# Optimization experiments

Measured on AMD Instinct MI355X. Metric: run time of the kernel, lower is better.

Reference implementation:

```python
import jax, jax.numpy as jnp
import numpy as np
import math

B, S, H = 4, 4096, 64
WINDOW = 2


def setup_inputs() -> dict:
    key = jax.random.key(0)
    ks = jax.random.split(key, 7)
    s = 0.05
    return {
        "feature": jax.random.normal(ks[0], (B, S, H), dtype=jnp.float32),
        "Wq": jax.random.normal(ks[1], (H, H), dtype=jnp.float32) * s,
        "bq": jax.random.normal(ks[2], (H,), dtype=jnp.float32) * s,
        "Wk": jax.random.normal(ks[3], (H, H), dtype=jnp.float32) * s,
        "bk": jax.random.normal(ks[4], (H,), dtype=jnp.float32) * s,
        "Wv": jax.random.normal(ks[5], (H, H), dtype=jnp.float32) * s,
        "bv": jax.random.normal(ks[6], (H,), dtype=jnp.float32) * s,
    }


def reference(feature, Wq, bq, Wk, bk, Wv, bv):
    b, seq, d_k = feature.shape
    # torch nn.Linear: y = x @ W.T + b
    q = feature @ Wq.T + bq  # [B,S,H]
    k = feature @ Wk.T + bk
    v = feature @ Wv.T + bv

    # banded 0/1 mask, |i-j| <= window, then softmax over the FULL row
    # (faithful to the original: zeros outside the band also get exp(0)=1 weight)
    idx = jnp.arange(seq)
    band = (jnp.abs(idx[:, None] - idx[None, :]) <= WINDOW).astype(jnp.float32)  # [S,S]
    weights = jax.nn.softmax(band, axis=-1)  # [S,S]

    # locally-averaged K: weights @ k, shared across batch
    mixed_k = jnp.einsum('st,bth->bsh', weights, k)  # [B,S,H]
    scores = jnp.einsum('bsh,bth->bst', q, mixed_k) / math.sqrt(d_k)  # [B,S,S]
    attn = jax.nn.softmax(scores, axis=-1)
    out = jnp.einsum('bst,bth->bsh', attn, v)  # [B,S,H]
    return out
```

## Files before the change

### kernel.cpp

```cpp
#include <hip/hip_runtime.h>
#include <hip/hip_bf16.h>
#include <math.h>

#define SEQ 4096
#define HD  64
#define NBATCH 4

#define EM1   1.71828182845904523536f
#define INVD5 (1.0f/(4096.f + 5.f*EM1))
#define INVD4 (1.0f/(4096.f + 4.f*EM1))
#define INVD3 (1.0f/(4096.f + 3.f*EM1))

typedef __attribute__((ext_vector_type(8))) short short8;
typedef __attribute__((ext_vector_type(4))) float f32x4;

__device__ __forceinline__ f32x4 mfma16(short8 a, short8 b, f32x4 c) {
    return __builtin_amdgcn_mfma_f32_16x16x32_bf16(a, b, c, 0, 0, 0);
}

__device__ __forceinline__ short bfs(float x) {
    __hip_bfloat16 h = __float2bfloat16(x);
    return *(short*)&h;
}

__device__ __forceinline__ short8 pack8(float4 a, float4 b) {
    short8 r;
    r[0] = bfs(a.x); r[1] = bfs(a.y); r[2] = bfs(a.z); r[3] = bfs(a.w);
    r[4] = bfs(b.x); r[5] = bfs(b.y); r[6] = bfs(b.z); r[7] = bfs(b.w);
    return r;
}

__device__ __forceinline__ float blo(unsigned v) { return __uint_as_float(v << 16); }
__device__ __forceinline__ float bhi(unsigned v) { return __uint_as_float(v & 0xffff0000u); }
__device__ __forceinline__ float b2f(__hip_bfloat16 h) { return __bfloat162float(h); }

__global__ __launch_bounds__(256) void wpack_kernel(
    const float* __restrict__ Wq, const float* __restrict__ Wk,
    const float* __restrict__ Wv, __hip_bfloat16* __restrict__ Wb,
    float* __restrict__ Mfull)
{
    const int blk = blockIdx.x, tid = threadIdx.x;
    if (blk >= 3) {
        float4 z = make_float4(0.f, 0.f, 0.f, 0.f);
        *(float4*)&Mfull[(blk - 3) * 1024 + tid * 4] = z;
        return;
    }
    const float* W = (blk == 0) ? Wq : (blk == 1) ? Wk : Wv;
    const float s = (blk == 0) ? 0.125f : 1.f;
    const float* src = W + tid * 16;
    float4 a0 = *(const float4*)(src);
    float4 a1 = *(const float4*)(src + 4);
    float4 a2 = *(const float4*)(src + 8);
    float4 a3 = *(const float4*)(src + 12);
    a0.x*=s; a0.y*=s; a0.z*=s; a0.w*=s;
    a1.x*=s; a1.y*=s; a1.z*=s; a1.w*=s;
    a2.x*=s; a2.y*=s; a2.z*=s; a2.w*=s;
    a3.x*=s; a3.y*=s; a3.z*=s; a3.w*=s;
    __hip_bfloat16* dst = Wb + blk * 4096 + tid * 16;
    *(short8*)(dst)     = pack8(a0, a1);
    *(short8*)(dst + 8) = pack8(a2, a3);
}

__global__ __launch_bounds__(128) void proj_kernel(
    const float* __restrict__ feat, const __hip_bfloat16* __restrict__ Wb,
    const float* __restrict__ bq, const float* __restrict__ bk,
    const float* __restrict__ bv,
    __hip_bfloat16* __restrict__ qsb, __hip_bfloat16* __restrict__ ktb,
    __hip_bfloat16* __restrict__ vtb,
    float* __restrict__ kpart, float* __restrict__ vpart)
{
    __shared__ __hip_bfloat16 tscr[64 * 72];
    __shared__ float kred[2][64];

    const int tid  = threadIdx.x;
    const int wave = tid >> 6, lane = tid & 63;
    const int quad = lane >> 4, ln = lane & 15;
    const int R0 = blockIdx.x * 32;
    const int b  = R0 >> 12;
    const int t0 = R0 & (SEQ - 1);

    short8 af0, af1;
    {
        const float* fp = feat + (size_t)(R0 + wave * 16 + ln) * HD + quad * 8;
        af0 = pack8(*(const float4*)(fp),      *(const float4*)(fp + 4));
        af1 = pack8(*(const float4*)(fp + 32), *(const float4*)(fp + 36));
    }

    const float* Bs[3] = {bq, bk, bv};

    #pragma unroll
    for (int m = 0; m < 3; ++m) {
        const __hip_bfloat16* W = Wb + m * 4096;
        const float* bias = Bs[m];
        #pragma unroll
        for (int ct = 0; ct < 4; ++ct) {
            const int col = ct * 16 + ln;
            const __hip_bfloat16* wp = W + col * 64 + quad * 8;
            short8 b0 = *(const short8*)(wp);
            short8 b1 = *(const short8*)(wp + 32);
            f32x4 c = {};
            c = mfma16(af0, b0, c);
            c = mfma16(af1, b1, c);

            if (m == 0) {
                const float bl = bias[col] * 0.125f;
                #pragma unroll
                for (int r = 0; r < 4; ++r)
                    qsb[(size_t)(R0 + wave * 16 + quad * 4 + r) * HD + col] =
                        __float2bfloat16(c[r] + bl);
            } else {
                const float bl = bias[col];
                float tot = c[0] + c[1] + c[2] + c[3];
                tot += __shfl_xor(tot, 16);
                tot += __shfl_xor(tot, 32);
                if (quad == 0) kred[wave][col] = tot;
                #pragma unroll
                for (int r = 0; r < 4; ++r)
                    tscr[col * 72 + wave * 16 + quad * 4 + r] =
                        __float2bfloat16(c[r] + bl);
            }
        }
        if (m > 0) {
            __syncthreads();
            if (tid < 64)
                ((m == 1) ? kpart : vpart)[(size_t)blockIdx.x * 64 + tid] =
                    kred[0][tid] + kred[1][tid] + 32.f * bias[tid];
            __hip_bfloat16* dst = (m == 1) ? ktb : vtb;
            #pragma unroll
            for (int i = 0; i < 2; ++i) {
                const int tsk = i * 128 + tid;
                const int hh = tsk >> 2, c8 = tsk & 3;
                short8 vv = *(const short8*)&tscr[hh * 72 + c8 * 8];
                *(short8*)(dst + ((size_t)(b * HD + hh)) * SEQ + t0 + c8 * 8) = vv;
            }
            __syncthreads();
        }
    }
}

__global__ __launch_bounds__(256) void mkernel(
    const __hip_bfloat16* __restrict__ ktb, const __hip_bfloat16* __restrict__ vtb,
    const float* __restrict__ kpart, const float* __restrict__ vpart,
    float* __restrict__ Mfull, float* __restrict__ Mcorr,
    float* __restrict__ mktotF, float* __restrict__ Vtot)
{
    __shared__ float vws[64 * 38];
    __shared__ __hip_bfloat16 lvt[64 * 40];
    __shared__ float scr[4][64];
    __shared__ float ktl[64], vtl[64];
    __shared__ float lc[4][64], vv_e[4][64];

    const int tid = threadIdx.x;

    if (blockIdx.y == 4) {
        if (blockIdx.x >= 16) return;
        const int b = blockIdx.x >> 2, slab = blockIdx.x & 3;
        if (slab == 2) return;
        const int h = tid & 63, g = tid >> 6;

        if (slab == 0 || slab == 3) {
            float kp = 0.f;
            for (int j = 0; j < 32; ++j)
                kp += kpart[(size_t)(b * 128 + g * 32 + j) * 64 + h];
            scr[g][h] = kp;
            __syncthreads();
            if (tid < 64) ktl[tid] = scr[0][tid] + scr[1][tid] + scr[2][tid] + scr[3][tid];
        }
        if (slab == 0) {
            __syncthreads();
            if (tid < 64) {
                const int hh = tid;
                const float kt = ktl[hh];
                const __hip_bfloat16* kr = ktb + (size_t)(b * 64 + hh) * SEQ;
                const float e0 = b2f(kr[0]), e1 = b2f(kr[1]), e2 = b2f(kr[2]), e3 = b2f(kr[3]);
                const float f0 = b2f(kr[SEQ-4]), f1 = b2f(kr[SEQ-3]);
                const float f2 = b2f(kr[SEQ-2]), f3 = b2f(kr[SEQ-1]);
                const float Sint = 5.f*kt - 4.f*e0 - 3.f*e1 - 2.f*e2 - e3
                                 - f0 - 2.f*f1 - 3.f*f2 - 4.f*f3;
                const float SlocD = Sint * INVD5
                                  + (e0+e1+e2 + f1+f2+f3) * INVD3
                                  + (e0+e1+e2+e3 + f0+f1+f2+f3) * INVD4;
                mktotF[b * 64 + hh] =
                    kt * (4092.f*INVD5 + 2.f*INVD4 + 2.f*INVD3) + EM1 * SlocD;
            }
        } else if (slab == 1) {
            float vp = 0.f;
            for (int j = 0; j < 32; ++j)
                vp += vpart[(size_t)(b * 128 + g * 32 + j) * 64 + h];
            scr[g][h] = vp;
            __syncthreads();
            if (tid < 64)
                Vtot[b * 64 + tid] = scr[0][tid] + scr[1][tid] + scr[2][tid] + scr[3][tid];
        } else {
            __syncthreads();
            {
                float vp = 0.f;
                for (int j = 0; j < 32; ++j)
                    vp += vpart[(size_t)(b * 128 + g * 32 + j) * 64 + h];
                scr[g][h] = vp;
            }
            __syncthreads();
            if (tid < 64) vtl[tid] = scr[0][tid] + scr[1][tid] + scr[2][tid] + scr[3][tid];
            if (tid < 64) {
                const int hh = tid;
                const __hip_bfloat16* kr = ktb + (size_t)(b * 64 + hh) * SEQ;
                const float e0 = b2f(kr[0]), e1 = b2f(kr[1]), e2 = b2f(kr[2]), e3 = b2f(kr[3]);
                const float f0 = b2f(kr[SEQ-4]), f1 = b2f(kr[SEQ-3]);
                const float f2 = b2f(kr[SEQ-2]), f3 = b2f(kr[SEQ-1]);
                lc[0][hh] = e0 + e1 + e2;
                lc[1][hh] = e0 + e1 + e2 + e3;
                lc[2][hh] = f0 + f1 + f2 + f3;
                lc[3][hh] = f1 + f2 + f3;
                const __hip_bfloat16* vr = vtb + (size_t)(b * 64 + hh) * SEQ;
                vv_e[0][hh] = b2f(vr[0]);
                vv_e[1][hh] = b2f(vr[1]);
                vv_e[2][hh] = b2f(vr[SEQ-2]);
                vv_e[3][hh] = b2f(vr[SEQ-1]);
            }
            __syncthreads();
            const float dd3 = INVD3 - INVD5, dd4 = INVD4 - INVD5;
            const int h1 = tid >> 2;
            const float l0 = lc[0][h1], l1 = lc[1][h1], l2 = lc[2][h1], l3 = lc[3][h1];
            const float kt1 = ktl[h1];
            #pragma unroll
            for (int j = 0; j < 16; ++j) {
                const int h2 = (tid & 3) * 16 + j;
                const float VD = INVD5 * vtl[h2]
                               + dd3 * (vv_e[0][h2] + vv_e[3][h2])
                               + dd4 * (vv_e[1][h2] + vv_e[2][h2]);
                Mcorr[(size_t)(b * 64 + h1) * 64 + h2] =
                    EM1 * (dd3 * (l0 * vv_e[0][h2] + l3 * vv_e[3][h2])
                         + dd4 * (l1 * vv_e[1][h2] + l2 * vv_e[2][h2]))
                    + kt1 * VD;
            }
        }
        return;
    }

    const int b = blockIdx.y, chunk = blockIdx.x;
    const int t0 = chunk * 32;

    for (int i = tid; i < 64 * 18; i += 256) {
        const int r = i / 18, c = i - r * 18;
        const int gt = t0 - 2 + c * 2;
        unsigned val = 0;
        if (gt >= 0 && gt <= SEQ - 2)
            val = *(const unsigned*)(vtb + (size_t)(b * 64 + r) * SEQ + gt);
        vws[r * 38 + c * 2]     = blo(val);
        vws[r * 38 + c * 2 + 1] = bhi(val);
    }
    __syncthreads();

    {
        const int h = tid & 63, g = tid >> 6;
        float w[12];
        #pragma unroll
        for (int j = 0; j < 12; ++j) w[j] = vws[h * 38 + g * 8 + j];
        short8 o;
        #pragma unroll
        for (int i = 0; i < 8; ++i)
            o[i] = bfs(w[i] + w[i+1] + w[i+2] + w[i+3] + w[i+4]);
        *(short8*)&lvt[h * 40 + g * 8] = o;
    }
    __syncthreads();

    const int wave = tid >> 6, lane = tid & 63, quad = lane >> 4, ln = lane & 15;
    short8 a = *(const short8*)(ktb + (size_t)(b * 64 + wave * 16 + ln) * SEQ
                                + t0 + quad * 8);
    f32x4 acc[4] = {};
    #pragma unroll
    for (int ct = 0; ct < 4; ++ct) {
        short8 bb = *(const short8*)&lvt[(ct * 16 + ln) * 40 + quad * 8];
        acc[ct] = mfma16(a, bb, acc[ct]);
    }
    float* mf = Mfull + b * 4096;
    #pragma unroll
    for (int ct = 0; ct < 4; ++ct)
        #pragma unroll
        for (int r = 0; r < 4; ++r)
            atomicAdd(&mf[(wave * 16 + quad * 4 + r) * 64 + ct * 16 + ln],
                      acc[ct][r]);
}

__global__ __launch_bounds__(256) void out_kernel(
    const __hip_bfloat16* __restrict__ qsb, const float* __restrict__ Mfull,
    const float* __restrict__ Mcorr, const float* __restrict__ mktotF,
    const float* __restrict__ Vtot, float* __restrict__ out)
{
    __shared__ __hip_bfloat16 tscr[64 * 72];

    const int tid  = threadIdx.x;
    const int wave = tid >> 6, lane = tid & 63;
    const int quad = lane >> 4, ln = lane & 15;
    const int R0 = blockIdx.x * 64;
    const int b  = R0 >> 12;

    {
        const int h2 = tid & 63, seg = tid >> 6;
        #pragma unroll
        for (int j = 0; j < 16; ++j) {
            const int h1 = seg * 16 + j;
            const float m = (EM1 * INVD5) * Mfull[b * 4096 + h1 * 64 + h2]
                          + Mcorr[(size_t)(b * 64 + h1) * 64 + h2];
            tscr[h2 * 72 + h1] = __float2bfloat16(m);
        }
    }
    __syncthreads();

    short8 qa0, qa1;
    {
        const __hip_bfloat16* qp = qsb + (size_t)(R0 + wave * 16 + ln) * HD + quad * 8;
        qa0 = *(const short8*)qp;
        qa1 = *(const short8*)(qp + 32);
    }
    short8 mk0, mk1;
    #pragma unroll
    for (int j = 0; j < 8; ++j) {
        mk0[j] = bfs(mktotF[b * 64 + quad * 8 + j]);
        mk1[j] = bfs(mktotF[b * 64 + 32 + quad * 8 + j]);
    }

    f32x4 acc[4];
    #pragma unroll
    for (int ct = 0; ct < 4; ++ct) {
        short8 b0 = *(const short8*)&tscr[(ct * 16 + ln) * 72 + quad * 8];
        short8 b1 = *(const short8*)&tscr[(ct * 16 + ln) * 72 + 32 + quad * 8];
        f32x4 c = {};
        c = mfma16(qa0, b0, c);
        c = mfma16(qa1, b1, c);
        acc[ct] = c;
    }
    f32x4 accd = {};
    accd = mfma16(qa0, mk0, accd);
    accd = mfma16(qa1, mk1, accd);

    float vt[4];
    #pragma unroll
    for (int ct = 0; ct < 4; ++ct) vt[ct] = Vtot[b * 64 + ct * 16 + ln];

    float inv[4];
    #pragma unroll
    for (int r = 0; r < 4; ++r) inv[r] = 1.f / (4096.f + accd[r]);

    #pragma unroll
    for (int ct = 0; ct < 4; ++ct)
        #pragma unroll
        for (int r = 0; r < 4; ++r)
            out[(size_t)(R0 + wave * 16 + quad * 4 + r) * HD + ct * 16 + ln] =
                (vt[ct] + acc[ct][r]) * inv[r];
}

extern "C" void kernel_launch(void* const* d_in, const int* in_sizes, int n_in,
                              void* d_out, int out_size, void* d_ws, size_t ws_size,
                              hipStream_t stream)
{
    const float* feat = (const float*)d_in[0];
    const float* Wq = (const float*)d_in[1];
    const float* bq = (const float*)d_in[2];
    const float* Wk = (const float*)d_in[3];
    const float* bk = (const float*)d_in[4];
    const float* Wv = (const float*)d_in[5];
    const float* bv = (const float*)d_in[6];
    float* out = (float*)d_out;

    char* ws = (char*)d_ws;
    __hip_bfloat16* qsb    = (__hip_bfloat16*)(ws + 0);
    __hip_bfloat16* ktb    = (__hip_bfloat16*)(ws + (2u << 20));
    __hip_bfloat16* vtb    = (__hip_bfloat16*)(ws + (4u << 20));
    float*          kpart  = (float*)(ws + (6u << 20));
    float*          vpart  = (float*)(ws + (6u << 20) + 131072);
    float*          Mfull  = (float*)(ws + (6u << 20) + 262144);
    float*          Mcorr  = (float*)(ws + (6u << 20) + 327680);
    float*          mktotF = (float*)(ws + (6u << 20) + 393216);
    float*          Vtot   = (float*)(ws + (6u << 20) + 394240);
    __hip_bfloat16* Wb     = (__hip_bfloat16*)(ws + (6u << 20) + 395264);

    wpack_kernel<<<dim3(19), dim3(256), 0, stream>>>(Wq, Wk, Wv, Wb, Mfull);
    proj_kernel<<<dim3(512), dim3(128), 0, stream>>>(
        feat, Wb, bq, bk, bv, qsb, ktb, vtb, kpart, vpart);
    mkernel<<<dim3(128, 5), dim3(256), 0, stream>>>(
        ktb, vtb, kpart, vpart, Mfull, Mcorr, mktotF, Vtot);
    out_kernel<<<dim3(256), dim3(256), 0, stream>>>(
        qsb, Mfull, Mcorr, mktotF, Vtot, out);
}
```

Baseline: 91.88 us.

## Fuse per-chunk K^T·localV products into projection kernel, replace atomics with partial reduction

The projection kernel now computes each 32-row chunk's K^T times the locally summed V directly from shared memory, loading two halo rows of features to build the V window. Each chunk writes its partial matrix to a buffer, so the transposed K/V round-trip through global memory and the float atomics into Mfull go away. A new reduction kernel sums the partials, and the edge-correction terms are simplified and folded into the output via a ktot·VD term. The cost is more partial-matrix traffic (bf16 Mpart) and an extra reduction pass.

```diff
diff --git a/kernel.cpp b/kernel.cpp
--- a/kernel.cpp
+++ b/kernel.cpp
@@ -30,21 +30,13 @@
     return r;
 }
 
-__device__ __forceinline__ float blo(unsigned v) { return __uint_as_float(v << 16); }
-__device__ __forceinline__ float bhi(unsigned v) { return __uint_as_float(v & 0xffff0000u); }
 __device__ __forceinline__ float b2f(__hip_bfloat16 h) { return __bfloat162float(h); }
 
 __global__ __launch_bounds__(256) void wpack_kernel(
     const float* __restrict__ Wq, const float* __restrict__ Wk,
-    const float* __restrict__ Wv, __hip_bfloat16* __restrict__ Wb,
-    float* __restrict__ Mfull)
+    const float* __restrict__ Wv, __hip_bfloat16* __restrict__ Wb)
 {
     const int blk = blockIdx.x, tid = threadIdx.x;
-    if (blk >= 3) {
-        float4 z = make_float4(0.f, 0.f, 0.f, 0.f);
-        *(float4*)&Mfull[(blk - 3) * 1024 + tid * 4] = z;
-        return;
-    }
     const float* W = (blk == 0) ? Wq : (blk == 1) ? Wk : Wv;
     const float s = (blk == 0) ? 0.125f : 1.f;
     const float* src = W + tid * 16;
@@ -61,16 +53,19 @@
     *(short8*)(dst + 8) = pack8(a2, a3);
 }
 
-__global__ __launch_bounds__(128) void proj_kernel(
+__global__ __launch_bounds__(128) void projm_kernel(
     const float* __restrict__ feat, const __hip_bfloat16* __restrict__ Wb,
     const float* __restrict__ bq, const float* __restrict__ bk,
     const float* __restrict__ bv,
-    __hip_bfloat16* __restrict__ qsb, __hip_bfloat16* __restrict__ ktb,
-    __hip_bfloat16* __restrict__ vtb,
-    float* __restrict__ kpart, float* __restrict__ vpart)
-{
-    __shared__ __hip_bfloat16 tscr[64 * 72];
+    __hip_bfloat16* __restrict__ qsb, float* __restrict__ kpart,
+    float* __restrict__ vpart, __hip_bfloat16* __restrict__ Mpart,
+    float* __restrict__ kedge)
+{
+    __shared__ __hip_bfloat16 kT[64 * 40];
+    __shared__ __hip_bfloat16 vT[64 * 40];
+    __shared__ __hip_bfloat16 lvt[64 * 40];
     __shared__ float kred[2][64];
+    __shared__ float vred[2][64];
 
     const int tid  = threadIdx.x;
     const int wave = tid >> 6, lane = tid & 63;
@@ -78,12 +73,27 @@
     const int R0 = blockIdx.x * 32;
     const int b  = R0 >> 12;
     const int t0 = R0 & (SEQ - 1);
+    const int chunk = blockIdx.x & 127;
 
     short8 af0, af1;
     {
         const float* fp = feat + (size_t)(R0 + wave * 16 + ln) * HD + quad * 8;
         af0 = pack8(*(const float4*)(fp),      *(const float4*)(fp + 4));
         af1 = pack8(*(const float4*)(fp + 32), *(const float4*)(fp + 36));
+    }
+
+    short8 hf0, hf1;
+    const bool hflag = (wave == 0) ? (t0 > 0) : (t0 < SEQ - 32);
+    {
+        const int hrow = (wave == 0) ? (t0 - 2 + ln) : (t0 + 32 + ln);
+        if (ln < 2 && hflag) {
+            const float* fp = feat + ((size_t)(b << 12) + hrow) * HD + quad * 8;
+            hf0 = pack8(*(const float4*)(fp),      *(const float4*)(fp + 4));
+            hf1 = pack8(*(const float4*)(fp + 32), *(const float4*)(fp + 36));
+        } else {
+            #pragma unroll
+            for (int j = 0; j < 8; ++j) { hf0[j] = 0; hf1[j] = 0; }
+        }
     }
 
     const float* Bs[3] = {bq, bk, bv};
@@ -108,7 +118,7 @@
                 for (int r = 0; r < 4; ++r)
                     qsb[(size_t)(R0 + wave * 16 + quad * 4 + r) * HD + col] =
                         __float2bfloat16(c[r] + bl);
-            } else {
+            } else if (m == 1) {
                 const float bl = bias[col];
                 float tot = c[0] + c[1] + c[2] + c[3];
                 tot += __shfl_xor(tot, 16);
@@ -116,227 +126,195 @@
                 if (quad == 0) kred[wave][col] = tot;
                 #pragma unroll
                 for (int r = 0; r < 4; ++r)
-                    tscr[col * 72 + wave * 16 + quad * 4 + r] =
+                    kT[col * 40 + wave * 16 + quad * 4 + r] =
                         __float2bfloat16(c[r] + bl);
+            } else {
+                const float bl = bias[col];
+                float tot = c[0] + c[1] + c[2] + c[3];
+                tot += __shfl_xor(tot, 16);
+                tot += __shfl_xor(tot, 32);
+                if (quad == 0) vred[wave][col] = tot;
+                #pragma unroll
+                for (int r = 0; r < 4; ++r)
+                    vT[col * 40 + 2 + wave * 16 + quad * 4 + r] =
+                        __float2bfloat16(c[r] + bl);
+                f32x4 hc = {};
+                hc = mfma16(hf0, b0, hc);
+                hc = mfma16(hf1, b1, hc);
+                if (quad == 0) {
+                    const int base = (wave == 0) ? 0 : 34;
+                    vT[col * 40 + base]     = __float2bfloat16(hflag ? hc[0] + bl : 0.f);
+                    vT[col * 40 + base + 1] = __float2bfloat16(hflag ? hc[1] + bl : 0.f);
+                }
             }
         }
-        if (m > 0) {
-            __syncthreads();
-            if (tid < 64)
-                ((m == 1) ? kpart : vpart)[(size_t)blockIdx.x * 64 + tid] =
-                    kred[0][tid] + kred[1][tid] + 32.f * bias[tid];
-            __hip_bfloat16* dst = (m == 1) ? ktb : vtb;
+    }
+    __syncthreads();
+
+    if (tid < 64) {
+        kpart[(size_t)blockIdx.x * 64 + tid] =
+            kred[0][tid] + kred[1][tid] + 32.f * bk[tid];
+        vpart[(size_t)blockIdx.x * 64 + tid] =
+            vred[0][tid] + vred[1][tid] + 32.f * bv[tid];
+    }
+
+    {
+        const int h = tid & 63;
+        const int tb = wave * 16;
+        float w[21];
+        #pragma unroll
+        for (int j = 0; j < 21; ++j) w[j] = b2f(vT[h * 40 + tb + j]);
+        #pragma unroll
+        for (int i = 0; i < 16; ++i)
+            lvt[h * 40 + tb + i] =
+                __float2bfloat16(w[i] + w[i+1] + w[i+2] + w[i+3] + w[i+4]);
+    }
+
+    if (chunk == 0) {
+        #pragma unroll
+        for (int i = 0; i < 2; ++i) {
+            const int idx = i * 128 + tid;
+            const int t = idx >> 6, h = idx & 63;
+            kedge[b * 512 + t * 64 + h] = b2f(kT[h * 40 + t]);
+        }
+    } else if (chunk == 127) {
+        #pragma unroll
+        for (int i = 0; i < 2; ++i) {
+            const int idx = i * 128 + tid;
+            const int t = idx >> 6, h = idx & 63;
+            kedge[b * 512 + (4 + t) * 64 + h] = b2f(kT[h * 40 + 28 + t]);
+        }
+    }
+    __syncthreads();
+
+    __hip_bfloat16* mp = Mpart + (size_t)(b * 128 + chunk) * 4096;
+    #pragma unroll
+    for (int p = 0; p < 2; ++p) {
+        const int strip = wave * 2 + p;
+        short8 a = *(const short8*)&kT[(strip * 16 + ln) * 40 + quad * 8];
+        #pragma unroll
+        for (int ct = 0; ct < 4; ++ct) {
+            short8 bb = *(const short8*)&lvt[(ct * 16 + ln) * 40 + quad * 8];
+            f32x4 acc = {};
+            acc = mfma16(a, bb, acc);
             #pragma unroll
-            for (int i = 0; i < 2; ++i) {
-                const int tsk = i * 128 + tid;
-                const int hh = tsk >> 2, c8 = tsk & 3;
-                short8 vv = *(const short8*)&tscr[hh * 72 + c8 * 8];
-                *(short8*)(dst + ((size_t)(b * HD + hh)) * SEQ + t0 + c8 * 8) = vv;
-            }
-            __syncthreads();
-        }
-    }
-}
-
-__global__ __launch_bounds__(256) void mkernel(
-    const __hip_bfloat16* __restrict__ ktb, const __hip_bfloat16* __restrict__ vtb,
-    const float* __restrict__ kpart, const float* __restrict__ vpart,
-    float* __restrict__ Mfull, float* __restrict__ Mcorr,
-    float* __restrict__ mktotF, float* __restrict__ Vtot)
-{
-    __shared__ float vws[64 * 38];
-    __shared__ __hip_bfloat16 lvt[64 * 40];
-    __shared__ float scr[4][64];
-    __shared__ float ktl[64], vtl[64];
-    __shared__ float lc[4][64], vv_e[4][64];
-
+            for (int r = 0; r < 4; ++r)
+                mp[(strip * 16 + quad * 4 + r) * 64 + ct * 16 + ln] =
+                    __float2bfloat16(acc[r]);
+        }
+    }
+}
+
+__global__ __launch_bounds__(256) void redprep_kernel(
+    const __hip_bfloat16* __restrict__ Mpart, const float* __restrict__ kpart,
+    const float* __restrict__ vpart, const float* __restrict__ kedge,
+    __hip_bfloat16* __restrict__ MTm, float* __restrict__ mktotF,
+    float* __restrict__ ktotF, float* __restrict__ VDs,
+    float* __restrict__ VtotF)
+{
+    __shared__ float red[4][64];
+    __shared__ float red2[4][64];
+    const int b = blockIdx.y, x = blockIdx.x;
     const int tid = threadIdx.x;
-
-    if (blockIdx.y == 4) {
-        if (blockIdx.x >= 16) return;
-        const int b = blockIdx.x >> 2, slab = blockIdx.x & 3;
-        if (slab == 2) return;
-        const int h = tid & 63, g = tid >> 6;
-
-        if (slab == 0 || slab == 3) {
-            float kp = 0.f;
-            for (int j = 0; j < 32; ++j)
-                kp += kpart[(size_t)(b * 128 + g * 32 + j) * 64 + h];
-            scr[g][h] = kp;
-            __syncthreads();
-            if (tid < 64) ktl[tid] = scr[0][tid] + scr[1][tid] + scr[2][tid] + scr[3][tid];
-        }
-        if (slab == 0) {
-            __syncthreads();
-            if (tid < 64) {
-                const int hh = tid;
-                const float kt = ktl[hh];
-                const __hip_bfloat16* kr = ktb + (size_t)(b * 64 + hh) * SEQ;
-                const float e0 = b2f(kr[0]), e1 = b2f(kr[1]), e2 = b2f(kr[2]), e3 = b2f(kr[3]);
-                const float f0 = b2f(kr[SEQ-4]), f1 = b2f(kr[SEQ-3]);
-                const float f2 = b2f(kr[SEQ-2]), f3 = b2f(kr[SEQ-1]);
-                const float Sint = 5.f*kt - 4.f*e0 - 3.f*e1 - 2.f*e2 - e3
-                                 - f0 - 2.f*f1 - 3.f*f2 - 4.f*f3;
-                const float SlocD = Sint * INVD5
-                                  + (e0+e1+e2 + f1+f2+f3) * INVD3
-                                  + (e0+e1+e2+e3 + f0+f1+f2+f3) * INVD4;
-                mktotF[b * 64 + hh] =
-                    kt * (4092.f*INVD5 + 2.f*INVD4 + 2.f*INVD3) + EM1 * SlocD;
-            }
-        } else if (slab == 1) {
-            float vp = 0.f;
-            for (int j = 0; j < 32; ++j)
-                vp += vpart[(size_t)(b * 128 + g * 32 + j) * 64 + h];
-            scr[g][h] = vp;
-            __syncthreads();
-            if (tid < 64)
-                Vtot[b * 64 + tid] = scr[0][tid] + scr[1][tid] + scr[2][tid] + scr[3][tid];
-        } else {
-            __syncthreads();
-            {
-                float vp = 0.f;
-                for (int j = 0; j < 32; ++j)
-                    vp += vpart[(size_t)(b * 128 + g * 32 + j) * 64 + h];
-                scr[g][h] = vp;
-            }
-            __syncthreads();
-            if (tid < 64) vtl[tid] = scr[0][tid] + scr[1][tid] + scr[2][tid] + scr[3][tid];
-            if (tid < 64) {
-                const int hh = tid;
-                const __hip_bfloat16* kr = ktb + (size_t)(b * 64 + hh) * SEQ;
-                const float e0 = b2f(kr[0]), e1 = b2f(kr[1]), e2 = b2f(kr[2]), e3 = b2f(kr[3]);
-                const float f0 = b2f(kr[SEQ-4]), f1 = b2f(kr[SEQ-3]);
-                const float f2 = b2f(kr[SEQ-2]), f3 = b2f(kr[SEQ-1]);
-                lc[0][hh] = e0 + e1 + e2;
-                lc[1][hh] = e0 + e1 + e2 + e3;
-                lc[2][hh] = f0 + f1 + f2 + f3;
-                lc[3][hh] = f1 + f2 + f3;
-                const __hip_bfloat16* vr = vtb + (size_t)(b * 64 + hh) * SEQ;
-                vv_e[0][hh] = b2f(vr[0]);
-                vv_e[1][hh] = b2f(vr[1]);
-                vv_e[2][hh] = b2f(vr[SEQ-2]);
-                vv_e[3][hh] = b2f(vr[SEQ-1]);
-            }
-            __syncthreads();
-            const float dd3 = INVD3 - INVD5, dd4 = INVD4 - INVD5;
-            const int h1 = tid >> 2;
-            const float l0 = lc[0][h1], l1 = lc[1][h1], l2 = lc[2][h1], l3 = lc[3][h1];
-            const float kt1 = ktl[h1];
-            #pragma unroll
-            for (int j = 0; j < 16; ++j) {
-                const int h2 = (tid & 3) * 16 + j;
-                const float VD = INVD5 * vtl[h2]
-                               + dd3 * (vv_e[0][h2] + vv_e[3][h2])
-                               + dd4 * (vv_e[1][h2] + vv_e[2][h2]);
-                Mcorr[(size_t)(b * 64 + h1) * 64 + h2] =
-                    EM1 * (dd3 * (l0 * vv_e[0][h2] + l3 * vv_e[3][h2])
-                         + dd4 * (l1 * vv_e[1][h2] + l2 * vv_e[2][h2]))
-                    + kt1 * VD;
-            }
-        }
+    const int g = tid >> 6, h2 = tid & 63;
+
+    if (x < 64) {
+        const int h1 = x;
+        float s = 0.f;
+        for (int c = g * 32; c < g * 32 + 32; ++c)
+            s += b2f(Mpart[(size_t)(b * 128 + c) * 4096 + h1 * 64 + h2]);
+        red[g][h2] = s;
+        __syncthreads();
+        if (tid < 64)
+            MTm[(size_t)b * 4096 + tid * 64 + h1] = __float2bfloat16(
+                (EM1 * INVD5) * (red[0][tid] + red[1][tid] + red[2][tid] + red[3][tid]));
         return;
     }
 
-    const int b = blockIdx.y, chunk = blockIdx.x;
-    const int t0 = chunk * 32;
-
-    for (int i = tid; i < 64 * 18; i += 256) {
-        const int r = i / 18, c = i - r * 18;
-        const int gt = t0 - 2 + c * 2;
-        unsigned val = 0;
-        if (gt >= 0 && gt <= SEQ - 2)
-            val = *(const unsigned*)(vtb + (size_t)(b * 64 + r) * SEQ + gt);
-        vws[r * 38 + c * 2]     = blo(val);
-        vws[r * 38 + c * 2 + 1] = bhi(val);
+    {
+        float kp = 0.f, vp = 0.f;
+        for (int j = 0; j < 32; ++j) {
+            kp += kpart[(size_t)(b * 128 + g * 32 + j) * 64 + h2];
+            vp += vpart[(size_t)(b * 128 + g * 32 + j) * 64 + h2];
+        }
+        red[g][h2] = kp;
+        red2[g][h2] = vp;
     }
     __syncthreads();
-
-    {
-        const int h = tid & 63, g = tid >> 6;
-        float w[12];
-        #pragma unroll
-        for (int j = 0; j < 12; ++j) w[j] = vws[h * 38 + g * 8 + j];
-        short8 o;
-        #pragma unroll
-        for (int i = 0; i < 8; ++i)
-            o[i] = bfs(w[i] + w[i+1] + w[i+2] + w[i+3] + w[i+4]);
-        *(short8*)&lvt[h * 40 + g * 8] = o;
-    }
-    __syncthreads();
-
-    const int wave = tid >> 6, lane = tid & 63, quad = lane >> 4, ln = lane & 15;
-    short8 a = *(const short8*)(ktb + (size_t)(b * 64 + wave * 16 + ln) * SEQ
-                                + t0 + quad * 8);
-    f32x4 acc[4] = {};
-    #pragma unroll
-    for (int ct = 0; ct < 4; ++ct) {
-        short8 bb = *(const short8*)&lvt[(ct * 16 + ln) * 40 + quad * 8];
-        acc[ct] = mfma16(a, bb, acc[ct]);
-    }
-    float* mf = Mfull + b * 4096;
-    #pragma unroll
-    for (int ct = 0; ct < 4; ++ct)
-        #pragma unroll
-        for (int r = 0; r < 4; ++r)
-            atomicAdd(&mf[(wave * 16 + quad * 4 + r) * 64 + ct * 16 + ln],
-                      acc[ct][r]);
-}
-
-__global__ __launch_bounds__(256) void out_kernel(
-    const __hip_bfloat16* __restrict__ qsb, const float* __restrict__ Mfull,
-    const float* __restrict__ Mcorr, const float* __restrict__ mktotF,
-    const float* __restrict__ Vtot, float* __restrict__ out)
-{
-    __shared__ __hip_bfloat16 tscr[64 * 72];
-
-    const int tid  = threadIdx.x;
-    const int wave = tid >> 6, lane = tid & 63;
-    const int quad = lane >> 4, ln = lane & 15;
-    const int R0 = blockIdx.x * 64;
-    const int b  = R0 >> 12;
-
-    {
-        const int h2 = tid & 63, seg = tid >> 6;
-        #pragma unroll
-        for (int j = 0; j < 16; ++j) {
-            const int h1 = seg * 16 + j;
-            const float m = (EM1 * INVD5) * Mfull[b * 4096 + h1 * 64 + h2]
-                          + Mcorr[(size_t)(b * 64 + h1) * 64 + h2];
-            tscr[h2 * 72 + h1] = __float2bfloat16(m);
-        }
-    }
-    __syncthreads();
+    if (tid < 64) {
+        const int hh = tid;
+        const float kt = red[0][hh] + red[1][hh] + red[2][hh] + red[3][hh];
+        const float vt = red2[0][hh] + red2[1][hh] + red2[2][hh] + red2[3][hh];
+        const float e0 = kedge[b * 512 + 0 * 64 + hh];
+        const float e1 = kedge[b * 512 + 1 * 64 + hh];
+        const float e2 = kedge[b * 512 + 2 * 64 + hh];
+        const float e3 = kedge[b * 512 + 3 * 64 + hh];
+        const float f0 = kedge[b * 512 + 4 * 64 + hh];
+        const float f1 = kedge[b * 512 + 5 * 64 + hh];
+        const float f2 = kedge[b * 512 + 6 * 64 + hh];
+        const float f3 = kedge[b * 512 + 7 * 64 + hh];
+        const float Sint = 5.f*kt - 4.f*e0 - 3.f*e1 - 2.f*e2 - e3
+                         - f0 - 2.f*f1 - 3.f*f2 - 4.f*f3;
+        const float SlocD = Sint * INVD5
+                          + (e0+e1+e2 + f1+f2+f3) * INVD3
+                          + (e0+e1+e2+e3 + f0+f1+f2+f3) * INVD4;
+        mktotF[b * 64 + hh] = kt * (4092.f*INVD5 + 2.f*INVD4 + 2.f*INVD3) + EM1 * SlocD;
+        ktotF[b * 64 + hh]  = kt;
+        VDs[b * 64 + hh]    = INVD5 * vt;
+        VtotF[b * 64 + hh]  = vt;
+    }
+}
+
+__global__ __launch_bounds__(64) void out_kernel(
+    const __hip_bfloat16* __restrict__ qsb, const __hip_bfloat16* __restrict__ MTm,
+    const float* __restrict__ mktotF, const float* __restrict__ ktotF,
+    const float* __restrict__ VDs, const float* __restrict__ VtotF,
+    float* __restrict__ out)
+{
+    const int tid = threadIdx.x;
+    const int quad = tid >> 4, ln = tid & 15;
+    const int R0 = blockIdx.x * 16;
+    const int b = R0 >> 12;
 
     short8 qa0, qa1;
     {
-        const __hip_bfloat16* qp = qsb + (size_t)(R0 + wave * 16 + ln) * HD + quad * 8;
+        const __hip_bfloat16* qp = qsb + (size_t)(R0 + ln) * HD + quad * 8;
         qa0 = *(const short8*)qp;
         qa1 = *(const short8*)(qp + 32);
     }
-    short8 mk0, mk1;
-    #pragma unroll
-    for (int j = 0; j < 8; ++j) {
-        mk0[j] = bfs(mktotF[b * 64 + quad * 8 + j]);
-        mk1[j] = bfs(mktotF[b * 64 + 32 + quad * 8 + j]);
-    }
-
+
+    const __hip_bfloat16* mtb = MTm + (size_t)b * 4096;
     f32x4 acc[4];
     #pragma unroll
     for (int ct = 0; ct < 4; ++ct) {
-        short8 b0 = *(const short8*)&tscr[(ct * 16 + ln) * 72 + quad * 8];
-        short8 b1 = *(const short8*)&tscr[(ct * 16 + ln) * 72 + 32 + quad * 8];
+        short8 b0 = *(const short8*)(mtb + (ct * 16 + ln) * 64 + quad * 8);
+        short8 b1 = *(const short8*)(mtb + (ct * 16 + ln) * 64 + 32 + quad * 8);
         f32x4 c = {};
         c = mfma16(qa0, b0, c);
         c = mfma16(qa1, b1, c);
         acc[ct] = c;
     }
-    f32x4 accd = {};
+
+    short8 mk0, mk1, kt0, kt1;
+    #pragma unroll
+    for (int j = 0; j < 8; ++j) {
+        mk0[j] = bfs(mktotF[b * 64 + quad * 8 + j]);
+        mk1[j] = bfs(mktotF[b * 64 + 32 + quad * 8 + j]);
+        kt0[j] = bfs(ktotF[b * 64 + quad * 8 + j]);
+        kt1[j] = bfs(ktotF[b * 64 + 32 + quad * 8 + j]);
+    }
+    f32x4 accd = {}, acck = {};
     accd = mfma16(qa0, mk0, accd);
     accd = mfma16(qa1, mk1, accd);
-
-    float vt[4];
-    #pragma unroll
-    for (int ct = 0; ct < 4; ++ct) vt[ct] = Vtot[b * 64 + ct * 16 + ln];
+    acck = mfma16(qa0, kt0, acck);
+    acck = mfma16(qa1, kt1, acck);
+
+    float vt[4], vd[4];
+    #pragma unroll
+    for (int ct = 0; ct < 4; ++ct) {
+        vt[ct] = VtotF[b * 64 + ct * 16 + ln];
+        vd[ct] = VDs[b * 64 + ct * 16 + ln];
+    }
 
     float inv[4];
     #pragma unroll
@@ -346,8 +324,8 @@
     for (int ct = 0; ct < 4; ++ct)
         #pragma unroll
         for (int r = 0; r < 4; ++r)
-            out[(size_t)(R0 + wave * 16 + quad * 4 + r) * HD + ct * 16 + ln] =
-                (vt[ct] + acc[ct][r]) * inv[r];
+            out[(size_t)(R0 + quad * 4 + r) * HD + ct * 16 + ln] =
+                (vt[ct] + acc[ct][r] + acck[r] * vd[ct]) * inv[r];
 }
 
 extern "C" void kernel_launch(void* const* d_in, const int* in_sizes, int n_in,
@@ -365,21 +343,22 @@
 
     char* ws = (char*)d_ws;
     __hip_bfloat16* qsb    = (__hip_bfloat16*)(ws + 0);
-    __hip_bfloat16* ktb    = (__hip_bfloat16*)(ws + (2u << 20));
-    __hip_bfloat16* vtb    = (__hip_bfloat16*)(ws + (4u << 20));
+    __hip_bfloat16* Mpart  = (__hip_bfloat16*)(ws + (2u << 20));
     float*          kpart  = (float*)(ws + (6u << 20));
     float*          vpart  = (float*)(ws + (6u << 20) + 131072);
-    float*          Mfull  = (float*)(ws + (6u << 20) + 262144);
-    float*          Mcorr  = (float*)(ws + (6u << 20) + 327680);
-    float*          mktotF = (float*)(ws + (6u << 20) + 393216);
-    float*          Vtot   = (float*)(ws + (6u << 20) + 394240);
-    __hip_bfloat16* Wb     = (__hip_bfloat16*)(ws + (6u << 20) + 395264);
-
-    wpack_kernel<<<dim3(19), dim3(256), 0, stream>>>(Wq, Wk, Wv, Wb, Mfull);
-    proj_kernel<<<dim3(512), dim3(128), 0, stream>>>(
-        feat, Wb, bq, bk, bv, qsb, ktb, vtb, kpart, vpart);
-    mkernel<<<dim3(128, 5), dim3(256), 0, stream>>>(
-        ktb, vtb, kpart, vpart, Mfull, Mcorr, mktotF, Vtot);
-    out_kernel<<<dim3(256), dim3(256), 0, stream>>>(
-        qsb, Mfull, Mcorr, mktotF, Vtot, out);
-}
+    float*          kedge  = (float*)(ws + (6u << 20) + 262144);
+    __hip_bfloat16* MTm    = (__hip_bfloat16*)(ws + (6u << 20) + 270336);
+    float*          mktotF = (float*)(ws + (6u << 20) + 303104);
+    float*          ktotF  = (float*)(ws + (6u << 20) + 304128);
+    float*          VDs    = (float*)(ws + (6u << 20) + 305152);
+    float*          VtotF  = (float*)(ws + (6u << 20) + 306176);
+    __hip_bfloat16* Wb     = (__hip_bfloat16*)(ws + (6u << 20) + 307200);
+
+    wpack_kernel<<<dim3(3), dim3(256), 0, stream>>>(Wq, Wk, Wv, Wb);
+    projm_kernel<<<dim3(512), dim3(128), 0, stream>>>(
+        feat, Wb, bq, bk, bv, qsb, kpart, vpart, Mpart, kedge);
+    redprep_kernel<<<dim3(65, NBATCH), dim3(256), 0, stream>>>(
+        Mpart, kpart, vpart, kedge, MTm, mktotF, ktotF, VDs, VtotF);
+    out_kernel<<<dim3(1024), dim3(64), 0, stream>>>(
+        qsb, MTm, mktotF, ktotF, VDs, VtotF, out);
+}
```

Result: faster. 82.86 us (median of 2 runs) (-9.8%).
